# Performance work log

Hardware: AMD Instinct MI355X
Metric: run time of the kernel (lower is better)

Reference implementation:

```python
import jax, jax.numpy as jnp
import numpy as np

D_MODEL = 1024
D_K = 1024
B, T = 4, 2048


def setup_inputs() -> dict:
    key = jax.random.key(0)
    kx, kq, kk, kv = jax.random.split(key, 4)
    s = 1.0 / np.sqrt(D_MODEL)
    return {
        "x": jax.random.normal(kx, (B, T, D_MODEL), dtype=jnp.float32),
        "W_q": jax.random.normal(kq, (D_MODEL, D_K), dtype=jnp.float32) * s,
        "W_k": jax.random.normal(kk, (D_MODEL, D_K), dtype=jnp.float32) * s,
        "W_v": jax.random.normal(kv, (D_MODEL, D_K), dtype=jnp.float32) * s,
    }


def reference(x, W_q, W_k, W_v):
    # x: (B, T, C); W_*: (C, d_k). Linear(no bias) == x @ W
    q = jnp.einsum('btc,ck->btk', x, W_q)
    k = jnp.einsum('btc,ck->btk', x, W_k)
    v = jnp.einsum('btc,ck->btk', x, W_v)
    d_k = W_q.shape[1]
    scores = jnp.einsum('bqk,bsk->bqs', q, k) / jnp.sqrt(jnp.asarray(d_k, x.dtype))
    T_ = x.shape[1]
    causal = jnp.tril(jnp.ones((T_, T_), dtype=bool))
    scores = jnp.where(causal, scores, jnp.asarray(-jnp.inf, scores.dtype))
    weights = jax.nn.softmax(scores, axis=-1)
    return jnp.einsum('bqs,bsk->bqk', weights, v)
```

## Files before the change

kernel.cpp:

```cpp
#include <hip/hip_runtime.h>
#include <hip/hip_bf16.h>
#include <stdint.h>
#include <math.h>

typedef __bf16 bf16x8 __attribute__((ext_vector_type(8)));
typedef float  f32x4  __attribute__((ext_vector_type(4)));
typedef unsigned int u32x4 __attribute__((ext_vector_type(4)));

__device__ __forceinline__ unsigned short f2bf(float x) {
    union { float f; unsigned u; } v; v.f = x;
    unsigned r = v.u + 0x7fffu + ((v.u >> 16) & 1u);
    return (unsigned short)(r >> 16);
}

__device__ __forceinline__ float bf2f(unsigned short b) {
    union { unsigned u; float f; } v; v.u = ((unsigned)b) << 16; return v.f;
}

__device__ __forceinline__ void async16(const void* g, void* l) {
    __builtin_amdgcn_global_load_lds(
        (const __attribute__((address_space(1))) void*)g,
        (__attribute__((address_space(3))) void*)l,
        16, 0, 0);
}

template <typename OutT, bool CAUSAL_SKIP, bool KLIMIT, bool VFOLD,
          bool XSWZ = false, bool TRIPACK = false>
__global__ __launch_bounds__(256, 4) void gemm_bt(
    const unsigned short* __restrict__ A,
    const unsigned short* __restrict__ Bt,
    OutT* __restrict__ C,
    unsigned short* __restrict__ VtOut,
    int M, int N, int K, int lda, int ldb, int ldc,
    int ldvt, int nsplit,
    long long sA, long long sB, long long sC, long long sVt, float scale)
{
    int bn, bm;
    if constexpr (TRIPACK) {
        const int o = blockIdx.x;
        const int chunk = (int)gridDim.x >> 3;
        const int t = (o & 7) * chunk + (o >> 3);
        int r = (int)((sqrtf(8.f * (float)t + 1.f) - 1.f) * 0.5f);
        while ((r + 1) * (r + 2) / 2 <= t) r++;
        while (r * (r + 1) / 2 > t) r--;
        bm = r; bn = t - r * (r + 1) / 2;
    } else if constexpr (XSWZ) {
        const int o = blockIdx.y * gridDim.x + blockIdx.x;
        const int x = o & 7, r = o >> 3;
        bn = x * 3 + (r % 3);
        bm = r / 3;
    } else {
        bn = blockIdx.x;
        bm = KLIMIT ? (gridDim.y - 1 - blockIdx.y) : blockIdx.y;
    }
    const int bz = blockIdx.z;
    if (CAUSAL_SKIP && bn > bm) return;

    A  += (long long)bz * sA;
    Bt += (long long)bz * sB;
    C  += (long long)bz * sC;

    const int m0 = bm * 128, n0 = bn * 128;
    const int Keff = KLIMIT ? min(K, (bm + 1) * 128) : K;

    __shared__ __align__(16) unsigned short LDS[2 * 2 * 128 * 32];

    const int tid  = threadIdx.x;
    const int w    = tid >> 6, l = tid & 63;
    const int wr   = w >> 1,  wc = w & 1;
    const int lrow = l & 15,  quad = l >> 4;

    f32x4 acc[4][4] = {};

    const int rA0  = 32 * w + (l >> 2);
    const int cOff = (((l & 3) ^ ((l >> 3) & 3))) * 8;
    const unsigned short* aG0 = A  + (long long)(m0 + rA0)      * lda + cOff;
    const unsigned short* aG1 = A  + (long long)(m0 + rA0 + 16) * lda + cOff;
    const unsigned short* bG0 = Bt + (long long)(n0 + rA0)      * ldb + cOff;
    const unsigned short* bG1 = Bt + (long long)(n0 + rA0 + 16) * ldb + cOff;
    unsigned short* aL = &LDS[(2 * w) * 512 + l * 8];
    unsigned short* bL = aL + 4096;

    const int sl = (lrow >> 1) & 3;

    async16(aG0, aL);
    async16(aG1, aL + 512);
    async16(bG0, bL);
    async16(bG1, bL + 512);

    for (int k0 = 0; k0 < Keff; k0 += 32) {
        const int cur = ((k0 >> 5) & 1) * 8192;
        __syncthreads();

        if (k0 + 32 < Keff) {
            const int nxt = cur ^ 8192;
            async16(aG0 + k0 + 32, aL + nxt);
            async16(aG1 + k0 + 32, aL + nxt + 512);
            async16(bG0 + k0 + 32, bL + nxt);
            async16(bG1 + k0 + 32, bL + nxt + 512);
        }

        const unsigned short* As = &LDS[cur];
        const unsigned short* Bs = &LDS[cur + 4096];
        bf16x8 af[4], bfr[4];
#pragma unroll
        for (int i = 0; i < 4; i++) {
            af[i]  = *(const bf16x8*)&As[(wr * 64 + i * 16 + lrow) * 32 + (quad ^ sl) * 8];
            bfr[i] = *(const bf16x8*)&Bs[(wc * 64 + i * 16 + lrow) * 32 + (quad ^ sl) * 8];
        }
#pragma unroll
        for (int i = 0; i < 4; i++)
#pragma unroll
            for (int j = 0; j < 4; j++)
                acc[i][j] = __builtin_amdgcn_mfma_f32_16x16x32_bf16(af[i], bfr[j], acc[i][j], 0, 0, 0);
    }

    if constexpr (VFOLD) {
        if (n0 >= nsplit) {
            unsigned short* Vp = VtOut + (long long)bz * sVt;
#pragma unroll
            for (int i = 0; i < 4; i++) {
                const int t = m0 + wr * 64 + i * 16 + quad * 4;
#pragma unroll
                for (int j = 0; j < 4; j++) {
                    const int d = (n0 - nsplit) + wc * 64 + j * 16 + lrow;
                    union { unsigned short u[4]; uint2 p; } o;
#pragma unroll
                    for (int r = 0; r < 4; r++) o.u[r] = f2bf(acc[i][j][r] * scale);
                    *(uint2*)(Vp + (long long)d * ldvt + t) = o.p;
                }
            }
            return;
        }
    }

    __syncthreads();

    char* eb = (char*)LDS + w * 2288;
    const int erow = l >> 2, ep = l & 3;

    if constexpr (sizeof(OutT) == 2) {
#pragma unroll
        for (int i = 0; i < 4; i++) {
#pragma unroll
            for (int j = 0; j < 4; j++)
#pragma unroll
                for (int r = 0; r < 4; r++)
                    *(unsigned short*)(eb + (quad * 4 + r) * 144 + (j * 16 + lrow) * 2) =
                        f2bf(acc[i][j][r] * scale);
            const long long gm = m0 + wr * 64 + i * 16 + erow;
#pragma unroll
            for (int c = 0; c < 2; c++) {
                u32x4 d = *(u32x4*)(eb + erow * 144 + ep * 32 + c * 16);
                *(u32x4*)((unsigned short*)C + gm * ldc + (n0 + wc * 64 + ep * 16 + c * 8)) = d;
            }
        }
    } else {
#pragma unroll
        for (int i = 0; i < 4; i++) {
            const long long gm = m0 + wr * 64 + i * 16 + erow;
#pragma unroll
            for (int jc = 0; jc < 2; jc++) {
#pragma unroll
                for (int jj = 0; jj < 2; jj++)
#pragma unroll
                    for (int r = 0; r < 4; r++)
                        *(float*)(eb + (quad * 4 + r) * 144 + (jj * 16 + lrow) * 4) =
                            acc[i][2 * jc + jj][r] * scale;
#pragma unroll
                for (int c = 0; c < 2; c++) {
                    f32x4 d = *(f32x4*)(eb + erow * 144 + ep * 32 + c * 16);
                    *(f32x4*)((float*)C + gm * ldc + (n0 + wc * 64 + jc * 32 + ep * 8 + c * 4)) = d;
                }
            }
        }
    }
}

__global__ __launch_bounds__(256) void cast_f32_bf16(
    const float4* __restrict__ in, unsigned short* __restrict__ out, int n4)
{
    int i = blockIdx.x * 256 + threadIdx.x;
    if (i >= n4) return;
    float4 v = in[i];
    union { unsigned short u[4]; uint2 p; } o;
    o.u[0] = f2bf(v.x); o.u[1] = f2bf(v.y); o.u[2] = f2bf(v.z); o.u[3] = f2bf(v.w);
    *(uint2*)(out + (long long)i * 4) = o.p;
}

__global__ __launch_bounds__(256) void transpose_cast_w3(
    const float* __restrict__ W0, const float* __restrict__ W1,
    const float* __restrict__ W2, unsigned short* __restrict__ out, int n)
{
    const float* in = (blockIdx.z == 0) ? W0 : (blockIdx.z == 1) ? W1 : W2;
    out += (long long)blockIdx.z * n * n;
    __shared__ float tile[32][33];
    const int tx = threadIdx.x, ty = threadIdx.y;
    const int c0 = blockIdx.x * 32, r0 = blockIdx.y * 32;
#pragma unroll
    for (int i = 0; i < 4; i++)
        tile[ty + i * 8][tx] = in[(long long)(r0 + ty + i * 8) * n + c0 + tx];
    __syncthreads();
#pragma unroll
    for (int i = 0; i < 4; i++)
        out[(long long)(c0 + ty + i * 8) * n + r0 + tx] = f2bf(tile[tx][ty + i * 8]);
}

__global__ __launch_bounds__(256) void causal_softmax_bf16(
    const unsigned short* __restrict__ S, unsigned short* __restrict__ P, int T)
{
    const int row = blockIdx.x;
    const int t   = row & (T - 1);
    const int L   = t + 1;
    const unsigned short* s = S + (long long)row * T;
    unsigned short* p = P + (long long)row * T;
    const int tid  = threadIdx.x;
    const int base = tid * 8;

    uint4 raw = *(const uint4*)(s + base);
    unsigned rr[4] = {raw.x, raw.y, raw.z, raw.w};
    float v[8];
#pragma unroll
    for (int k = 0; k < 4; k++) {
        union { unsigned u; float f; } a, b;
        a.u = (rr[k] & 0xFFFFu) << 16;
        b.u = rr[k] & 0xFFFF0000u;
        v[2 * k] = a.f; v[2 * k + 1] = b.f;
    }
    float mx = -3.0e38f;
#pragma unroll
    for (int k = 0; k < 8; k++) {
        if (base + k >= L) v[k] = -3.0e38f;
        mx = fmaxf(mx, v[k]);
    }
#pragma unroll
    for (int off = 32; off; off >>= 1) mx = fmaxf(mx, __shfl_xor(mx, off));
    __shared__ float red[4], red2[4];
    const int wid = tid >> 6, lid = tid & 63;
    if (lid == 0) red[wid] = mx;
    __syncthreads();
    mx = fmaxf(fmaxf(red[0], red[1]), fmaxf(red[2], red[3]));

    float sum = 0.f;
#pragma unroll
    for (int k = 0; k < 8; k++) { v[k] = __expf(v[k] - mx); sum += v[k]; }
#pragma unroll
    for (int off = 32; off; off >>= 1) sum += __shfl_xor(sum, off);
    if (lid == 0) red2[wid] = sum;
    __syncthreads();
    sum = red2[0] + red2[1] + red2[2] + red2[3];
    const float inv = 1.0f / sum;

    union { unsigned short u[8]; uint4 q; } o;
#pragma unroll
    for (int k = 0; k < 8; k++) o.u[k] = f2bf(v[k] * inv);
    *(uint4*)(p + base) = o.q;
}

extern "C" void kernel_launch(void* const* d_in, const int* in_sizes, int n_in,
                              void* d_out, int out_size, void* d_ws, size_t ws_size,
                              hipStream_t stream)
{
    const int B = 4, T = 2048, C = 1024, D = 1024;
    const float* x  = (const float*)d_in[0];
    const float* Wq = (const float*)d_in[1];
    const float* Wk = (const float*)d_in[2];
    const float* Wv = (const float*)d_in[3];
    float* out = (float*)d_out;
    char* ws = (char*)d_ws;

    const size_t MB = 1ull << 20;
    unsigned short* Xbf   = (unsigned short*)(ws + 0);
    unsigned short* WqkvT = (unsigned short*)(ws + 16 * MB);
    unsigned short* QK    = (unsigned short*)(ws + 22 * MB);
    unsigned short* Vt    = (unsigned short*)(ws + 54 * MB);
    unsigned short* Sbf   = (unsigned short*)(ws + 70 * MB);
    unsigned short* P     = (unsigned short*)(ws + 0);

    const long long sX  = (long long)T * C;
    const long long sQK = (long long)T * 2 * D;
    const long long sVt = (long long)D * T;
    const long long sS  = (long long)T * T;
    const long long sO  = (long long)T * D;

    {
        int n4 = B * T * C / 4;
        cast_f32_bf16<<<dim3((n4 + 255) / 256), dim3(256), 0, stream>>>(
            (const float4*)x, Xbf, n4);
    }
    {
        dim3 g(32, 32, 3), b(32, 8);
        transpose_cast_w3<<<g, b, 0, stream>>>(Wq, Wk, Wv, WqkvT, 1024);
    }
    {
        dim3 g(3072 / 128, 2048 / 128, 4), b(256);
        gemm_bt<unsigned short, false, false, true, true><<<g, b, 0, stream>>>(
            Xbf, WqkvT, QK, Vt, 2048, 3072, 1024, 1024, 1024, 2048,
             T,  2048, sX, 0, sQK, sVt, 1.0f);
    }
    {
        dim3 g(136, 1, 4), b(256);
        gemm_bt<unsigned short, false, false, false, false, true><<<g, b, 0, stream>>>(
            QK, QK + D, Sbf, nullptr, 2048, 2048, 1024, 2 * D, 2 * D, 2048,
            0, 0, sQK, sQK, sS, 0, 0.03125f);
    }
    {
        causal_softmax_bf16<<<dim3(B * T), dim3(256), 0, stream>>>(Sbf, P, T);
    }
    {
        dim3 g(1024 / 128, 2048 / 128, 4), b(256);
        gemm_bt<float, false, true, false><<<g, b, 0, stream>>>(
            P, Vt, out, nullptr, 2048, 1024, 2048, 2048, 2048, 1024,
            0, 0, sS, sVt, sO, 0, 1.0f);
    }
    (void)in_sizes; (void)n_in; (void)out_size; (void)ws_size;
}
```

Measured before the change: 244.8 us.

## Remap GEMM block indices so each XCD handles one batch's tiles

Replaces the per-GEMM tile swizzles with a unified ZMODE scheme that maps the low three bits of the block index (the XCD round-robin slot) to a batch, and spreads that batch's tiles across the launch. All three GEMMs (QKV projection, QK^T triangle, PV) now use flattened grids with this mapping. The aim is to keep each batch's operands resident in one XCD's L2 and improve cache reuse. The PV GEMM keeps its descending-row order so the longest K ranges start first.

```diff
diff --git a/kernel.cpp b/kernel.cpp
--- a/kernel.cpp
+++ b/kernel.cpp
@@ -24,8 +24,7 @@
         16, 0, 0);
 }
 
-template <typename OutT, bool CAUSAL_SKIP, bool KLIMIT, bool VFOLD,
-          bool XSWZ = false, bool TRIPACK = false>
+template <typename OutT, bool KLIMIT, bool VFOLD, int ZMODE>
 __global__ __launch_bounds__(256, 4) void gemm_bt(
     const unsigned short* __restrict__ A,
     const unsigned short* __restrict__ Bt,
@@ -35,26 +34,30 @@
     int ldvt, int nsplit,
     long long sA, long long sB, long long sC, long long sVt, float scale)
 {
-    int bn, bm;
-    if constexpr (TRIPACK) {
-        const int o = blockIdx.x;
-        const int chunk = (int)gridDim.x >> 3;
-        const int t = (o & 7) * chunk + (o >> 3);
+    int bn, bm, bz;
+    if constexpr (ZMODE == 1) {
+        const int o = blockIdx.x, x = o & 7, q = o >> 3;
+        bz = x >> 1;
+        const int tile = (x & 1) * 192 + q * 4 + blockIdx.z;
+        bn = tile / 16; bm = tile % 16;
+    } else if constexpr (ZMODE == 2) {
+        const int o = blockIdx.x, x = o & 7, q = o >> 3;
+        bz = x >> 1;
+        const int t = (x & 1) * 68 + q * 4 + blockIdx.z;
         int r = (int)((sqrtf(8.f * (float)t + 1.f) - 1.f) * 0.5f);
         while ((r + 1) * (r + 2) / 2 <= t) r++;
         while (r * (r + 1) / 2 > t) r--;
         bm = r; bn = t - r * (r + 1) / 2;
-    } else if constexpr (XSWZ) {
-        const int o = blockIdx.y * gridDim.x + blockIdx.x;
-        const int x = o & 7, r = o >> 3;
-        bn = x * 3 + (r % 3);
-        bm = r / 3;
+    } else if constexpr (ZMODE == 3) {
+        const int o = blockIdx.x, x = o & 7, q = o >> 3;
+        bz = x >> 1;
+        const int tile = (x & 1) * 64 + q * 4 + blockIdx.z;
+        bn = tile >> 4; bm = 15 - (tile & 15);
     } else {
         bn = blockIdx.x;
         bm = KLIMIT ? (gridDim.y - 1 - blockIdx.y) : blockIdx.y;
-    }
-    const int bz = blockIdx.z;
-    if (CAUSAL_SKIP && bn > bm) return;
+        bz = blockIdx.z;
+    }
 
     A  += (long long)bz * sA;
     Bt += (long long)bz * sB;
@@ -293,14 +296,14 @@
         transpose_cast_w3<<<g, b, 0, stream>>>(Wq, Wk, Wv, WqkvT, 1024);
     }
     {
-        dim3 g(3072 / 128, 2048 / 128, 4), b(256);
-        gemm_bt<unsigned short, false, false, true, true><<<g, b, 0, stream>>>(
+        dim3 g(384, 1, 4), b(256);
+        gemm_bt<unsigned short, false, true, 1><<<g, b, 0, stream>>>(
             Xbf, WqkvT, QK, Vt, 2048, 3072, 1024, 1024, 1024, 2048,
              T,  2048, sX, 0, sQK, sVt, 1.0f);
     }
     {
         dim3 g(136, 1, 4), b(256);
-        gemm_bt<unsigned short, false, false, false, false, true><<<g, b, 0, stream>>>(
+        gemm_bt<unsigned short, false, false, 2><<<g, b, 0, stream>>>(
             QK, QK + D, Sbf, nullptr, 2048, 2048, 1024, 2 * D, 2 * D, 2048,
             0, 0, sQK, sQK, sS, 0, 0.03125f);
     }
@@ -308,8 +311,8 @@
         causal_softmax_bf16<<<dim3(B * T), dim3(256), 0, stream>>>(Sbf, P, T);
     }
     {
-        dim3 g(1024 / 128, 2048 / 128, 4), b(256);
-        gemm_bt<float, false, true, false><<<g, b, 0, stream>>>(
+        dim3 g(128, 1, 4), b(256);
+        gemm_bt<float, true, false, 3><<<g, b, 0, stream>>>(
             P, Vt, out, nullptr, 2048, 1024, 2048, 2048, 2048, 1024,
             0, 0, sS, sVt, sO, 0, 1.0f);
     }
```

New measurement: 236.8 us. -3.3%, faster.
